# Kernel tuning notes

Hardware: AMD Instinct MI355X
Metric: run time of the kernel (lower is better)

Reference implementation:

```python
import jax, jax.numpy as jnp
import numpy as np

BATCH, D, H = 8192, 512, 2048
DT = 0.1
N_STEPS = 10  # t0=0.0 -> t1=1.0 with dt0=0.1, ConstantStepSize


def setup_inputs() -> dict:
    key = jax.random.key(0)
    k0, k1, k2 = jax.random.split(key, 3)
    y0 = jax.random.normal(k0, (BATCH, D), dtype=jnp.float32)
    # fan-in scaled init to keep the tanh MLP vector field well-conditioned
    W1 = jax.random.normal(k1, (D, H), dtype=jnp.float32) / np.sqrt(D).astype(np.float32)
    b1 = jnp.zeros((H,), dtype=jnp.float32)
    W2 = jax.random.normal(k2, (H, D), dtype=jnp.float32) / np.sqrt(H).astype(np.float32)
    b2 = jnp.zeros((D,), dtype=jnp.float32)
    return {"y0": y0, "W1": W1, "b1": b1, "W2": W2, "b2": b2}


def reference(y0, W1, b1, W2, b2):
    dt = jnp.float32(DT)

    def f(t, y):  # autonomous MLP vector field; t unused but kept for ODE form
        return jnp.tanh(y @ W1 + b1) @ W2 + b2

    def heun_step(y, t):
        k1 = f(t, y)
        k2 = f(t + dt, y + dt * k1)
        return y + (0.5 * dt) * (k1 + k2), None

    ts = jnp.arange(N_STEPS, dtype=jnp.float32) * dt
    y1, _ = jax.lax.scan(heun_step, y0, ts)
    return y1  # solution.ys[0] at t1=1.0
```

## Files before the change

### kernel.cpp

```cpp
#include <hip/hip_runtime.h>
#include <hip/hip_bf16.h>
#include <cstdint>


#define BATCHN 8192
#define DDIM 512
#define HDIM 2048
#define CW 512
#define NCH (HDIM / CW)

typedef short short8 __attribute__((ext_vector_type(8)));
typedef float floatx16 __attribute__((ext_vector_type(16)));

__device__ __forceinline__ unsigned short f2bf(float f) {
  union { __hip_bfloat16 h; unsigned short u; } cv;
  cv.h = __float2bfloat16(f);
  return cv.u;
}

__device__ __forceinline__ float fast_tanh(float x) {
  float e = __expf(2.0f * x);
  return 1.0f - 2.0f / (e + 1.0f);
}

__device__ __forceinline__ void glds16(const void* g, void* l) {
  __builtin_amdgcn_global_load_lds(
      (const __attribute__((address_space(1))) void*)(uintptr_t)g,
      (__attribute__((address_space(3))) void*)(uint32_t)(uintptr_t)l,
      16, 0, 0);
}


__global__ __launch_bounds__(1024, 4) void fused_feval(
    const unsigned short* __restrict__ yPack,
    const unsigned short* __restrict__ w1p,
    const unsigned short* __restrict__ w2p,
    const float* __restrict__ b1,
    const float* __restrict__ b2,
    const float* __restrict__ stateIn,
    float* __restrict__ stateOut,
    unsigned short* __restrict__ outPack,
    int epi) {
  __shared__ unsigned short yA[32 * 512];
  __shared__ unsigned short hA[2][32 * 512];

  const int tid  = threadIdx.x;
  const int lane = tid & 63;
  const int w    = tid >> 6;
  const int c31  = lane & 31;
  const int lhi  = lane >> 5;
  const int blk  = blockIdx.x;
  const int B0   = blk * 32;

  {
    const unsigned short* src = yPack + (size_t)blk * (32 * 512);
    glds16(src + (size_t)tid * 8, &yA[tid * 8]);
    glds16(src + (size_t)(1024 + tid) * 8, &yA[(1024 + tid) * 8]);
  }

  float bb1v[NCH];
#pragma unroll
  for (int c = 0; c < NCH; ++c) bb1v[c] = b1[c * CW + w * 32 + c31];

  __syncthreads();

  floatx16 accY = {};

#pragma unroll
  for (int c = 0; c < NCH; ++c) {
    floatx16 acc1 = {};
    const unsigned short* w1b =
        w1p + ((size_t)((c * 16 + w) * 32) * 64 + lane) * 8;
#pragma unroll
    for (int ks = 0; ks < 32; ++ks) {
      short8 a = *(const short8*)&yA[(ks * 64 + lane) * 8];
      short8 b = *(const short8*)(w1b + (size_t)ks * 512);
      acc1 = __builtin_amdgcn_mfma_f32_32x32x16_bf16(a, b, acc1, 0, 0, 0);
    }

    {
      unsigned short* hbuf = hA[c & 1];
      const int kloc = w * 32 + c31;
      const float bb = bb1v[c];
      const int ksf = kloc >> 4;
      const int lh  = (kloc >> 3) & 1;
      const int jj  = kloc & 7;
      const int mhi = lhi * 4;
#pragma unroll
      for (int reg = 0; reg < 16; ++reg) {
        const int m = (reg & 3) + 8 * (reg >> 2) + mhi;
        hbuf[(ksf * 64 + (m + 32 * lh)) * 8 + jj] =
            f2bf(fast_tanh(acc1[reg] + bb));
      }
    }

    if (c > 0) {
      const int cc = c - 1;
      const unsigned short* hp = hA[cc & 1];
      const unsigned short* w2b =
          w2p + ((size_t)(w * 128 + cc * 32) * 64 + lane) * 8;
#pragma unroll
      for (int ks = 0; ks < 32; ++ks) {
        short8 a = *(const short8*)&hp[(ks * 64 + lane) * 8];
        short8 b = *(const short8*)(w2b + (size_t)ks * 512);
        accY = __builtin_amdgcn_mfma_f32_32x32x16_bf16(a, b, accY, 0, 0, 0);
      }
    }
    __syncthreads();
  }
  {
    const int cc = NCH - 1;
    const unsigned short* hp = hA[cc & 1];
    const unsigned short* w2b =
        w2p + ((size_t)(w * 128 + cc * 32) * 64 + lane) * 8;
#pragma unroll
    for (int ks = 0; ks < 32; ++ks) {
      short8 a = *(const short8*)&hp[(ks * 64 + lane) * 8];
      short8 b = *(const short8*)(w2b + (size_t)ks * 512);
      accY = __builtin_amdgcn_mfma_f32_32x32x16_bf16(a, b, accY, 0, 0, 0);
    }
  }
  __syncthreads();

  {
    unsigned short* pbuf = &hA[0][0];
    const int ncol = w * 32 + c31;
    const float bb = b2[ncol];
    const int ksf = ncol >> 4;
    const int lh  = (ncol >> 3) & 1;
    const int jj  = ncol & 7;
    const int mhi = lhi * 4;
#pragma unroll
    for (int reg = 0; reg < 16; ++reg) {
      const int mrow = (reg & 3) + 8 * (reg >> 2) + mhi;
      const int row = B0 + mrow;
      const size_t idx = (size_t)row * DDIM + ncol;
      const float v = accY[reg] + bb;
      float nv;
      if (epi == 1) {
        const float y = stateIn[idx];
        stateOut[idx] = y + 0.05f * v;
        nv = y + 0.1f * v;
      } else {
        const float yn = stateIn[idx] + 0.05f * v;
        stateOut[idx] = yn;
        nv = yn;
      }
      pbuf[(ksf * 64 + (mrow + 32 * lh)) * 8 + jj] = f2bf(nv);
    }
    __syncthreads();
    unsigned short* dst = outPack + (size_t)blk * (32 * 512);
#pragma unroll
    for (int p = 0; p < 2; ++p) {
      short8 v = *(const short8*)&pbuf[(size_t)(p * 1024 + tid) * 8];
      *(short8*)&dst[(size_t)(p * 1024 + tid) * 8] = v;
    }
  }
}

__global__ void pack_b(const float* __restrict__ src, unsigned short* __restrict__ dst,
                       int KB, int N) {
  const int t = blockIdx.x * 256 + threadIdx.x;
  const int lane = t & 63, f = t >> 6;
  const int nb = f / KB, kb = f % KB;
  const int k0 = kb * 16 + (lane >> 5) * 8, n = nb * 32 + (lane & 31);
  short8 v;
#pragma unroll
  for (int j = 0; j < 8; ++j)
    v[j] = (short)f2bf(src[(size_t)(k0 + j) * N + n]);
  *(short8*)&dst[(size_t)t * 8] = v;
}

__global__ void pack_y(const float* __restrict__ y0, float* __restrict__ yF,
                       unsigned short* __restrict__ ypk) {
  const int t = blockIdx.x * 256 + threadIdx.x;
  const int lane = t & 63, f = t >> 6;
  const int rb = f >> 5, ks = f & 31;
  const int row = rb * 32 + (lane & 31), c0 = ks * 16 + (lane >> 5) * 8;
  short8 v;
#pragma unroll
  for (int j = 0; j < 8; ++j) {
    const float x = y0[(size_t)row * DDIM + c0 + j];
    yF[(size_t)row * DDIM + c0 + j] = x;
    v[j] = (short)f2bf(x);
  }
  *(short8*)&ypk[(size_t)t * 8] = v;
}

extern "C" void kernel_launch(void* const* d_in, const int* in_sizes, int n_in,
                              void* d_out, int out_size, void* d_ws, size_t ws_size,
                              hipStream_t stream) {
  const float* y0 = (const float*)d_in[0];
  const float* W1 = (const float*)d_in[1];
  const float* b1 = (const float*)d_in[2];
  const float* W2 = (const float*)d_in[3];
  const float* b2 = (const float*)d_in[4];

  char* ws = (char*)d_ws;
  float*          yF   = (float*)(ws);
  float*          pF   = (float*)(ws + (size_t)(16u << 20));
  unsigned short* ypk  = (unsigned short*)(ws + (size_t)(32u << 20));
  unsigned short* ympk = (unsigned short*)(ws + (size_t)(40u << 20));
  unsigned short* w1p  = (unsigned short*)(ws + (size_t)(48u << 20));
  unsigned short* w2p  = (unsigned short*)(ws + (size_t)(50u << 20));

  pack_b<<<512, 256, 0, stream>>>(W1, w1p, 32, HDIM);
  pack_b<<<512, 256, 0, stream>>>(W2, w2p, 128, DDIM);
  pack_y<<<2048, 256, 0, stream>>>(y0, yF, ypk);

  const dim3 grid(256), blkd(1024);
  for (int s = 0; s < 10; ++s) {
    fused_feval<<<grid, blkd, 0, stream>>>(ypk, w1p, w2p, b1, b2, yF, pF, ympk, 1);
    float* yOut = (s == 9) ? (float*)d_out : yF;
    fused_feval<<<grid, blkd, 0, stream>>>(ympk, w1p, w2p, b1, b2, pF, yOut, ypk, 2);
  }
}
```

Before: 1.113 ms.

## Halve block to 8 waves computing two N-tiles each with register-prefetched weights

Each block now uses 512 threads (8 waves) instead of 1024, and each wave computes two 32-wide output column tiles. The LDS A-fragment is reused across both MFMAs, which halves LDS reads per MFMA. The weight B-fragments are prefetched into registers in double-buffered groups of 8 k-steps to hide global load latency. The cost is much higher register pressure (two accumulator sets plus 32 prefetched short8 fragments), and there are fewer waves per block to hide latency.

```diff
diff --git a/kernel.cpp b/kernel.cpp
--- a/kernel.cpp
+++ b/kernel.cpp
@@ -31,7 +31,7 @@
 }
 
 
-__global__ __launch_bounds__(1024, 4) void fused_feval(
+__global__ __launch_bounds__(512, 2) void fused_feval(
     const unsigned short* __restrict__ yPack,
     const unsigned short* __restrict__ w1p,
     const unsigned short* __restrict__ w2p,
@@ -54,56 +54,101 @@
 
   {
     const unsigned short* src = yPack + (size_t)blk * (32 * 512);
-    glds16(src + (size_t)tid * 8, &yA[tid * 8]);
-    glds16(src + (size_t)(1024 + tid) * 8, &yA[(1024 + tid) * 8]);
-  }
-
-  float bb1v[NCH];
-#pragma unroll
-  for (int c = 0; c < NCH; ++c) bb1v[c] = b1[c * CW + w * 32 + c31];
+#pragma unroll
+    for (int p = 0; p < 4; ++p)
+      glds16(src + (size_t)(p * 512 + tid) * 8, &yA[(p * 512 + tid) * 8]);
+  }
+
+  float bb1v[NCH][2];
+#pragma unroll
+  for (int c = 0; c < NCH; ++c)
+#pragma unroll
+    for (int i = 0; i < 2; ++i)
+      bb1v[c][i] = b1[c * CW + (w * 2 + i) * 32 + c31];
 
   __syncthreads();
 
-  floatx16 accY = {};
+  floatx16 accY[2] = {};
 
 #pragma unroll
   for (int c = 0; c < NCH; ++c) {
-    floatx16 acc1 = {};
-    const unsigned short* w1b =
-        w1p + ((size_t)((c * 16 + w) * 32) * 64 + lane) * 8;
-#pragma unroll
-    for (int ks = 0; ks < 32; ++ks) {
-      short8 a = *(const short8*)&yA[(ks * 64 + lane) * 8];
-      short8 b = *(const short8*)(w1b + (size_t)ks * 512);
-      acc1 = __builtin_amdgcn_mfma_f32_32x32x16_bf16(a, b, acc1, 0, 0, 0);
+    floatx16 acc1[2] = {};
+    const unsigned short* w1b0 =
+        w1p + ((size_t)((c * 16 + w * 2 + 0) * 32) * 64 + lane) * 8;
+    const unsigned short* w1b1 =
+        w1p + ((size_t)((c * 16 + w * 2 + 1) * 32) * 64 + lane) * 8;
+    short8 bb[2][2][8];
+#pragma unroll
+    for (int k = 0; k < 8; ++k) {
+      bb[0][0][k] = *(const short8*)(w1b0 + (size_t)k * 512);
+      bb[0][1][k] = *(const short8*)(w1b1 + (size_t)k * 512);
+    }
+#pragma unroll
+    for (int h = 0; h < 4; ++h) {
+      const int cur = h & 1;
+      if (h < 3) {
+#pragma unroll
+        for (int k = 0; k < 8; ++k) {
+          bb[cur ^ 1][0][k] = *(const short8*)(w1b0 + (size_t)((h + 1) * 8 + k) * 512);
+          bb[cur ^ 1][1][k] = *(const short8*)(w1b1 + (size_t)((h + 1) * 8 + k) * 512);
+        }
+      }
+#pragma unroll
+      for (int k = 0; k < 8; ++k) {
+        short8 a = *(const short8*)&yA[((h * 8 + k) * 64 + lane) * 8];
+        acc1[0] = __builtin_amdgcn_mfma_f32_32x32x16_bf16(a, bb[cur][0][k], acc1[0], 0, 0, 0);
+        acc1[1] = __builtin_amdgcn_mfma_f32_32x32x16_bf16(a, bb[cur][1][k], acc1[1], 0, 0, 0);
+      }
     }
 
     {
       unsigned short* hbuf = hA[c & 1];
-      const int kloc = w * 32 + c31;
-      const float bb = bb1v[c];
-      const int ksf = kloc >> 4;
-      const int lh  = (kloc >> 3) & 1;
-      const int jj  = kloc & 7;
-      const int mhi = lhi * 4;
-#pragma unroll
-      for (int reg = 0; reg < 16; ++reg) {
-        const int m = (reg & 3) + 8 * (reg >> 2) + mhi;
-        hbuf[(ksf * 64 + (m + 32 * lh)) * 8 + jj] =
-            f2bf(fast_tanh(acc1[reg] + bb));
+#pragma unroll
+      for (int i1 = 0; i1 < 2; ++i1) {
+        const int kloc = (w * 2 + i1) * 32 + c31;
+        const float bb1 = bb1v[c][i1];
+        const int ksf = kloc >> 4;
+        const int lh  = (kloc >> 3) & 1;
+        const int jj  = kloc & 7;
+        const int mhi = lhi * 4;
+#pragma unroll
+        for (int reg = 0; reg < 16; ++reg) {
+          const int m = (reg & 3) + 8 * (reg >> 2) + mhi;
+          hbuf[(ksf * 64 + (m + 32 * lh)) * 8 + jj] =
+              f2bf(fast_tanh(acc1[i1][reg] + bb1));
+        }
       }
     }
 
     if (c > 0) {
       const int cc = c - 1;
       const unsigned short* hp = hA[cc & 1];
-      const unsigned short* w2b =
-          w2p + ((size_t)(w * 128 + cc * 32) * 64 + lane) * 8;
-#pragma unroll
-      for (int ks = 0; ks < 32; ++ks) {
-        short8 a = *(const short8*)&hp[(ks * 64 + lane) * 8];
-        short8 b = *(const short8*)(w2b + (size_t)ks * 512);
-        accY = __builtin_amdgcn_mfma_f32_32x32x16_bf16(a, b, accY, 0, 0, 0);
+      const unsigned short* w2b0 =
+          w2p + ((size_t)((w * 2 + 0) * 128 + cc * 32) * 64 + lane) * 8;
+      const unsigned short* w2b1 =
+          w2p + ((size_t)((w * 2 + 1) * 128 + cc * 32) * 64 + lane) * 8;
+      short8 cb[2][2][8];
+#pragma unroll
+      for (int k = 0; k < 8; ++k) {
+        cb[0][0][k] = *(const short8*)(w2b0 + (size_t)k * 512);
+        cb[0][1][k] = *(const short8*)(w2b1 + (size_t)k * 512);
+      }
+#pragma unroll
+      for (int h = 0; h < 4; ++h) {
+        const int cur = h & 1;
+        if (h < 3) {
+#pragma unroll
+          for (int k = 0; k < 8; ++k) {
+            cb[cur ^ 1][0][k] = *(const short8*)(w2b0 + (size_t)((h + 1) * 8 + k) * 512);
+            cb[cur ^ 1][1][k] = *(const short8*)(w2b1 + (size_t)((h + 1) * 8 + k) * 512);
+          }
+        }
+#pragma unroll
+        for (int k = 0; k < 8; ++k) {
+          short8 a = *(const short8*)&hp[((h * 8 + k) * 64 + lane) * 8];
+          accY[0] = __builtin_amdgcn_mfma_f32_32x32x16_bf16(a, cb[cur][0][k], accY[0], 0, 0, 0);
+          accY[1] = __builtin_amdgcn_mfma_f32_32x32x16_bf16(a, cb[cur][1][k], accY[1], 0, 0, 0);
+        }
       }
     }
     __syncthreads();
@@ -111,49 +156,71 @@
   {
     const int cc = NCH - 1;
     const unsigned short* hp = hA[cc & 1];
-    const unsigned short* w2b =
-        w2p + ((size_t)(w * 128 + cc * 32) * 64 + lane) * 8;
-#pragma unroll
-    for (int ks = 0; ks < 32; ++ks) {
-      short8 a = *(const short8*)&hp[(ks * 64 + lane) * 8];
-      short8 b = *(const short8*)(w2b + (size_t)ks * 512);
-      accY = __builtin_amdgcn_mfma_f32_32x32x16_bf16(a, b, accY, 0, 0, 0);
+    const unsigned short* w2b0 =
+        w2p + ((size_t)((w * 2 + 0) * 128 + cc * 32) * 64 + lane) * 8;
+    const unsigned short* w2b1 =
+        w2p + ((size_t)((w * 2 + 1) * 128 + cc * 32) * 64 + lane) * 8;
+    short8 cb[2][2][8];
+#pragma unroll
+    for (int k = 0; k < 8; ++k) {
+      cb[0][0][k] = *(const short8*)(w2b0 + (size_t)k * 512);
+      cb[0][1][k] = *(const short8*)(w2b1 + (size_t)k * 512);
+    }
+#pragma unroll
+    for (int h = 0; h < 4; ++h) {
+      const int cur = h & 1;
+      if (h < 3) {
+#pragma unroll
+        for (int k = 0; k < 8; ++k) {
+          cb[cur ^ 1][0][k] = *(const short8*)(w2b0 + (size_t)((h + 1) * 8 + k) * 512);
+          cb[cur ^ 1][1][k] = *(const short8*)(w2b1 + (size_t)((h + 1) * 8 + k) * 512);
+        }
+      }
+#pragma unroll
+      for (int k = 0; k < 8; ++k) {
+        short8 a = *(const short8*)&hp[((h * 8 + k) * 64 + lane) * 8];
+        accY[0] = __builtin_amdgcn_mfma_f32_32x32x16_bf16(a, cb[cur][0][k], accY[0], 0, 0, 0);
+        accY[1] = __builtin_amdgcn_mfma_f32_32x32x16_bf16(a, cb[cur][1][k], accY[1], 0, 0, 0);
+      }
     }
   }
   __syncthreads();
 
   {
     unsigned short* pbuf = &hA[0][0];
-    const int ncol = w * 32 + c31;
-    const float bb = b2[ncol];
-    const int ksf = ncol >> 4;
-    const int lh  = (ncol >> 3) & 1;
-    const int jj  = ncol & 7;
-    const int mhi = lhi * 4;
-#pragma unroll
-    for (int reg = 0; reg < 16; ++reg) {
-      const int mrow = (reg & 3) + 8 * (reg >> 2) + mhi;
-      const int row = B0 + mrow;
-      const size_t idx = (size_t)row * DDIM + ncol;
-      const float v = accY[reg] + bb;
-      float nv;
-      if (epi == 1) {
-        const float y = stateIn[idx];
-        stateOut[idx] = y + 0.05f * v;
-        nv = y + 0.1f * v;
-      } else {
-        const float yn = stateIn[idx] + 0.05f * v;
-        stateOut[idx] = yn;
-        nv = yn;
-      }
-      pbuf[(ksf * 64 + (mrow + 32 * lh)) * 8 + jj] = f2bf(nv);
+#pragma unroll
+    for (int i = 0; i < 2; ++i) {
+      const int ncol = (w * 2 + i) * 32 + c31;
+      const float bb = b2[ncol];
+      const int ksf = ncol >> 4;
+      const int lh  = (ncol >> 3) & 1;
+      const int jj  = ncol & 7;
+      const int mhi = lhi * 4;
+#pragma unroll
+      for (int reg = 0; reg < 16; ++reg) {
+        const int mrow = (reg & 3) + 8 * (reg >> 2) + mhi;
+        const int row = B0 + mrow;
+        const size_t idx = (size_t)row * DDIM + ncol;
+        const float v = accY[i][reg] + bb;
+        float nv;
+        if (epi == 1) {
+          const float y = stateIn[idx];
+          stateOut[idx] = y + 0.05f * v;
+          nv = y + 0.1f * v;
+        } else {
+          const float yn = stateIn[idx] + 0.05f * v;
+          stateOut[idx] = yn;
+          nv = yn;
+        }
+        pbuf[(ksf * 64 + (mrow + 32 * lh)) * 8 + jj] = f2bf(nv);
+      }
     }
     __syncthreads();
     unsigned short* dst = outPack + (size_t)blk * (32 * 512);
 #pragma unroll
-    for (int p = 0; p < 2; ++p) {
-      short8 v = *(const short8*)&pbuf[(size_t)(p * 1024 + tid) * 8];
-      *(short8*)&dst[(size_t)(p * 1024 + tid) * 8] = v;
+    for (int p = 0; p < 4; ++p) {
+      short8 v = *(const short8*)&pbuf[(size_t)(p * 512 + tid) * 8];
+      *(short8*)&dst[(size_t)(p * 512 + tid) * 8] = v;
     }
   }
 }
@@ -208,7 +275,7 @@
   pack_b<<<512, 256, 0, stream>>>(W2, w2p, 128, DDIM);
   pack_y<<<2048, 256, 0, stream>>>(y0, yF, ypk);
 
-  const dim3 grid(256), blkd(1024);
+  const dim3 grid(256), blkd(512);
   for (int s = 0; s < 10; ++s) {
     fused_feval<<<grid, blkd, 0, stream>>>(ypk, w1p, w2p, b1, b2, yF, pF, ympk, 1);
     float* yOut = (s == 9) ? (float*)d_out : yF;
```

Result: slower. 1.159 ms (+4.1%).

## Quantize second GEMM to int8 with per-column weight scales

Applied to the files above, without the earlier changes.

Moves the hidden-to-output GEMM from bf16 MFMA to int8 MFMA. The tanh activations are quantized to int8 with a fixed scale of 127, and W2 gets symmetric per-column scales computed by new column-max and pack kernels. The intent is to double MFMA throughput and halve LDS and weight traffic for the second matmul. The cost is added quantization error in the ODE integration, which could exceed tolerance, plus a few extra preprocessing kernels.

```diff
diff --git a/kernel.cpp b/kernel.cpp
--- a/kernel.cpp
+++ b/kernel.cpp
@@ -11,6 +11,8 @@
 
 typedef short short8 __attribute__((ext_vector_type(8)));
 typedef float floatx16 __attribute__((ext_vector_type(16)));
+typedef int int4v __attribute__((ext_vector_type(4)));
+typedef int intx16 __attribute__((ext_vector_type(16)));
 
 __device__ __forceinline__ unsigned short f2bf(float f) {
   union { __hip_bfloat16 h; unsigned short u; } cv;
@@ -23,18 +25,12 @@
   return 1.0f - 2.0f / (e + 1.0f);
 }
 
-__device__ __forceinline__ void glds16(const void* g, void* l) {
-  __builtin_amdgcn_global_load_lds(
-      (const __attribute__((address_space(1))) void*)(uintptr_t)g,
-      (__attribute__((address_space(3))) void*)(uint32_t)(uintptr_t)l,
-      16, 0, 0);
-}
-
 
 __global__ __launch_bounds__(1024, 4) void fused_feval(
     const unsigned short* __restrict__ yPack,
     const unsigned short* __restrict__ w1p,
-    const unsigned short* __restrict__ w2p,
+    const signed char* __restrict__ w2p8,
+    const float* __restrict__ qsArr,
     const float* __restrict__ b1,
     const float* __restrict__ b2,
     const float* __restrict__ stateIn,
@@ -42,7 +38,7 @@
     unsigned short* __restrict__ outPack,
     int epi) {
   __shared__ unsigned short yA[32 * 512];
-  __shared__ unsigned short hA[2][32 * 512];
+  __shared__ signed char hA8[2][32 * CW];
 
   const int tid  = threadIdx.x;
   const int lane = tid & 63;
@@ -54,8 +50,14 @@
 
   {
     const unsigned short* src = yPack + (size_t)blk * (32 * 512);
-    glds16(src + (size_t)tid * 8, &yA[tid * 8]);
-    glds16(src + (size_t)(1024 + tid) * 8, &yA[(1024 + tid) * 8]);
+    __builtin_amdgcn_global_load_lds(
+        (const __attribute__((address_space(1))) void*)(uintptr_t)(src + (size_t)tid * 8),
+        (__attribute__((address_space(3))) void*)(uint32_t)(uintptr_t)&yA[tid * 8],
+        16, 0, 0);
+    __builtin_amdgcn_global_load_lds(
+        (const __attribute__((address_space(1))) void*)(uintptr_t)(src + (size_t)(1024 + tid) * 8),
+        (__attribute__((address_space(3))) void*)(uint32_t)(uintptr_t)&yA[(1024 + tid) * 8],
+        16, 0, 0);
   }
 
   float bb1v[NCH];
@@ -64,7 +66,7 @@
 
   __syncthreads();
 
-  floatx16 accY = {};
+  intx16 accY = {};
 
 #pragma unroll
   for (int c = 0; c < NCH; ++c) {
@@ -79,52 +81,52 @@
     }
 
     {
-      unsigned short* hbuf = hA[c & 1];
-      const int kloc = w * 32 + c31;
+      signed char* hbuf = hA8[c & 1];
       const float bb = bb1v[c];
-      const int ksf = kloc >> 4;
-      const int lh  = (kloc >> 3) & 1;
-      const int jj  = kloc & 7;
+      const int khalf = (c31 >> 4) << 5;
+      const int jj8 = c31 & 15;
       const int mhi = lhi * 4;
 #pragma unroll
       for (int reg = 0; reg < 16; ++reg) {
         const int m = (reg & 3) + 8 * (reg >> 2) + mhi;
-        hbuf[(ksf * 64 + (m + 32 * lh)) * 8 + jj] =
-            f2bf(fast_tanh(acc1[reg] + bb));
+        const float hv = fast_tanh(acc1[reg] + bb);
+        hbuf[(w * 64 + khalf + m) * 16 + jj8] =
+            (signed char)(int)rintf(hv * 127.0f);
       }
     }
 
     if (c > 0) {
       const int cc = c - 1;
-      const unsigned short* hp = hA[cc & 1];
-      const unsigned short* w2b =
-          w2p + ((size_t)(w * 128 + cc * 32) * 64 + lane) * 8;
-#pragma unroll
-      for (int ks = 0; ks < 32; ++ks) {
-        short8 a = *(const short8*)&hp[(ks * 64 + lane) * 8];
-        short8 b = *(const short8*)(w2b + (size_t)ks * 512);
-        accY = __builtin_amdgcn_mfma_f32_32x32x16_bf16(a, b, accY, 0, 0, 0);
+      const signed char* hp = hA8[cc & 1];
+      const signed char* w2b =
+          w2p8 + ((size_t)(w * 64 + cc * 16) * 64 + lane) * 16;
+#pragma unroll
+      for (int ks = 0; ks < 16; ++ks) {
+        int4v a = *(const int4v*)&hp[(ks * 64 + lane) * 16];
+        int4v b = *(const int4v*)(w2b + (size_t)ks * 1024);
+        accY = __builtin_amdgcn_mfma_i32_32x32x32_i8(a, b, accY, 0, 0, 0);
       }
     }
     __syncthreads();
   }
   {
     const int cc = NCH - 1;
-    const unsigned short* hp = hA[cc & 1];
-    const unsigned short* w2b =
-        w2p + ((size_t)(w * 128 + cc * 32) * 64 + lane) * 8;
-#pragma unroll
-    for (int ks = 0; ks < 32; ++ks) {
-      short8 a = *(const short8*)&hp[(ks * 64 + lane) * 8];
-      short8 b = *(const short8*)(w2b + (size_t)ks * 512);
-      accY = __builtin_amdgcn_mfma_f32_32x32x16_bf16(a, b, accY, 0, 0, 0);
+    const signed char* hp = hA8[cc & 1];
+    const signed char* w2b =
+        w2p8 + ((size_t)(w * 64 + cc * 16) * 64 + lane) * 16;
+#pragma unroll
+    for (int ks = 0; ks < 16; ++ks) {
+      int4v a = *(const int4v*)&hp[(ks * 64 + lane) * 16];
+      int4v b = *(const int4v*)(w2b + (size_t)ks * 1024);
+      accY = __builtin_amdgcn_mfma_i32_32x32x32_i8(a, b, accY, 0, 0, 0);
     }
   }
   __syncthreads();
 
   {
-    unsigned short* pbuf = &hA[0][0];
+    unsigned short* pbuf = (unsigned short*)&hA8[0][0];
     const int ncol = w * 32 + c31;
+    const float sc = qsArr[ncol] * (1.0f / 127.0f);
     const float bb = b2[ncol];
     const int ksf = ncol >> 4;
     const int lh  = (ncol >> 3) & 1;
@@ -135,7 +137,7 @@
       const int mrow = (reg & 3) + 8 * (reg >> 2) + mhi;
       const int row = B0 + mrow;
       const size_t idx = (size_t)row * DDIM + ncol;
-      const float v = accY[reg] + bb;
+      const float v = (float)accY[reg] * sc + bb;
       float nv;
       if (epi == 1) {
         const float y = stateIn[idx];
@@ -171,6 +173,35 @@
   *(short8*)&dst[(size_t)t * 8] = v;
 }
 
+__global__ void zero_cm(unsigned* __restrict__ cm) { cm[threadIdx.x] = 0u; }
+
+__global__ void colmax_w2(const float* __restrict__ w2, unsigned* __restrict__ cm) {
+  const int n = threadIdx.x;
+  const int k0 = blockIdx.x * 16;
+  float m = 0.0f;
+#pragma unroll
+  for (int i = 0; i < 16; ++i) m = fmaxf(m, fabsf(w2[(size_t)(k0 + i) * DDIM + n]));
+  atomicMax(&cm[n], __float_as_uint(m));
+}
+
+__global__ void pack_w2i8(const float* __restrict__ w2, const unsigned* __restrict__ cm,
+                          signed char* __restrict__ dst, float* __restrict__ qsArr) {
+  const int t = blockIdx.x * 256 + threadIdx.x;
+  const int lane = t & 63, f = t >> 6;
+  const int nb = f >> 6, kb = f & 63;
+  const int n = nb * 32 + (lane & 31);
+  const int k0 = kb * 32 + (lane >> 5) * 16;
+  float qs = __uint_as_float(cm[n]) * (1.0f / 127.0f);
+  if (qs <= 0.0f) qs = 1.0f;
+  if (kb == 0 && (lane >> 5) == 0) qsArr[n] = qs;
+  const float inv = 1.0f / qs;
+  union { signed char b[16]; int4v v; } o;
+#pragma unroll
+  for (int j = 0; j < 16; ++j)
+    o.b[j] = (signed char)(int)rintf(w2[(size_t)(k0 + j) * DDIM + n] * inv);
+  *(int4v*)&dst[(size_t)t * 16] = o.v;
+}
+
 __global__ void pack_y(const float* __restrict__ y0, float* __restrict__ yF,
                        unsigned short* __restrict__ ypk) {
   const int t = blockIdx.x * 256 + threadIdx.x;
@@ -202,16 +233,20 @@
   unsigned short* ypk  = (unsigned short*)(ws + (size_t)(32u << 20));
   unsigned short* ympk = (unsigned short*)(ws + (size_t)(40u << 20));
   unsigned short* w1p  = (unsigned short*)(ws + (size_t)(48u << 20));
-  unsigned short* w2p  = (unsigned short*)(ws + (size_t)(50u << 20));
-
+  signed char*    w2p8 = (signed char*)(ws + (size_t)(50u << 20));
+  float*          qsArr = (float*)(ws + (size_t)(51u << 20));
+  unsigned*       cmU   = (unsigned*)(ws + (size_t)(51u << 20) + 4096);
+
+  zero_cm<<<1, 512, 0, stream>>>(cmU);
+  colmax_w2<<<128, 512, 0, stream>>>(W2, cmU);
   pack_b<<<512, 256, 0, stream>>>(W1, w1p, 32, HDIM);
-  pack_b<<<512, 256, 0, stream>>>(W2, w2p, 128, DDIM);
+  pack_w2i8<<<256, 256, 0, stream>>>(W2, cmU, w2p8, qsArr);
   pack_y<<<2048, 256, 0, stream>>>(y0, yF, ypk);
 
   const dim3 grid(256), blkd(1024);
   for (int s = 0; s < 10; ++s) {
-    fused_feval<<<grid, blkd, 0, stream>>>(ypk, w1p, w2p, b1, b2, yF, pF, ympk, 1);
+    fused_feval<<<grid, blkd, 0, stream>>>(ypk, w1p, w2p8, qsArr, b1, b2, yF, pF, ympk, 1);
     float* yOut = (s == 9) ? (float*)d_out : yF;
-    fused_feval<<<grid, blkd, 0, stream>>>(ympk, w1p, w2p, b1, b2, pF, yOut, ypk, 2);
-  }
-}
+    fused_feval<<<grid, blkd, 0, stream>>>(ympk, w1p, w2p8, qsArr, b1, b2, pF, yOut, ypk, 2);
+  }
+}
```

Result: faster. 988.9 us (-11.2%).
